# Kernel optimization log

Measured on AMD Instinct MI355X. Metric: run time of the kernel, lower is better.

The kernel has to match this reference:

```python
import jax, jax.numpy as jnp
import numpy as np

B, S, D = 2, 2048, 512
E, K = 8, 2
H = 4 * D  # expert_dim
EPS = 1e-10


def setup_inputs() -> dict:
    key = jax.random.key(0)
    ks = jax.random.split(key, 5)
    scale = 1.0 / np.sqrt(D)
    return {
        "x": jax.random.normal(ks[0], (B, S, D), dtype=jnp.float32),
        "w_router": jax.random.normal(ks[1], (D, E), dtype=jnp.float32) * scale,
        "w_gate": jax.random.normal(ks[2], (D, E * H), dtype=jnp.float32) * scale,
        "w_up": jax.random.normal(ks[3], (D, E * H), dtype=jnp.float32) * scale,
        "w_down": jax.random.normal(ks[4], (H, D), dtype=jnp.float32) * (1.0 / np.sqrt(H)),
    }


def reference(x, w_router, w_gate, w_up, w_down):
    b, s, d = x.shape
    n = b * s
    xf = x.reshape(n, d)

    # Router: softmax over experts, pick top-k, renormalize
    router_probs = jax.nn.softmax(xf @ w_router, axis=-1)          # [N, E]
    top_p, top_i = jax.lax.top_k(router_probs, K)                  # [N, K]
    top_p = top_p / (top_p.sum(axis=-1, keepdims=True) + EPS)

    # Dense all-expert gate/up projections (as in original module)
    gate = jax.nn.silu(xf @ w_gate).reshape(n, E, H)               # [N, E, H]
    up = (xf @ w_up).reshape(n, E, H)                              # [N, E, H]

    # Gather per-token top-k expert slices and combine
    sel_gate = jnp.take_along_axis(gate, top_i[:, :, None], axis=1)  # [N, K, H]
    sel_up = jnp.take_along_axis(up, top_i[:, :, None], axis=1)      # [N, K, H]
    combined = jnp.sum(top_p[:, :, None] * sel_gate * sel_up, axis=1)  # [N, H]

    out = (combined @ w_down).reshape(b, s, d)

    # Load-balancing aux loss
    expert_probs = router_probs.mean(axis=0)                       # [E]
    lb_loss = E * jnp.sum(expert_probs * jnp.log(expert_probs * E + EPS))
    return out, lb_loss
```

## Files before the change

kernel.cpp:

```cpp
#include <hip/hip_runtime.h>
#include <hip/hip_bf16.h>

#define N_TOK 4096
#define D_DIM 512
#define E_NUM 8
#define H_DIM 2048

typedef __attribute__((ext_vector_type(8))) short short8;
typedef __attribute__((ext_vector_type(4))) float f32x4;

__device__ inline short f2bs(float f) {
  __hip_bfloat16 h = __float2bfloat16(f);
  return *reinterpret_cast<short*>(&h);
}

__device__ inline void llds16(const short* g, short* l) {
  __builtin_amdgcn_global_load_lds(
      (const __attribute__((address_space(1))) void*)g,
      (__attribute__((address_space(3))) void*)l, 16, 0, 0);
}

__global__ void __launch_bounds__(256) prep_kernel(
    const float* __restrict__ wg, const float* __restrict__ wu,
    const float* __restrict__ wd, short* __restrict__ wgb,
    short* __restrict__ wub, short* __restrict__ wdb,
    float* __restrict__ out, int* __restrict__ e_cnt,
    float* __restrict__ loss_acc, int* __restrict__ loss_cnt) {
  int u = blockIdx.x;
  int tid = threadIdx.x;
  if (u < 17408) {
    __shared__ float tbuf[32][33];
    const float* in;
    short* op;
    int R, C, c0, r0;
    if (u < 16384) {
      in = (u < 8192) ? wg : wu;
      op = (u < 8192) ? wgb : wub;
      int v = u & 8191;
      R = D_DIM; C = E_NUM * H_DIM;
      c0 = (v & 511) * 32; r0 = (v >> 9) * 32;
    } else {
      in = wd; op = wdb;
      int v = u - 16384;
      R = H_DIM; C = D_DIM;
      c0 = (v & 15) * 32; r0 = (v >> 4) * 32;
    }
    int tx = tid & 31, ty = tid >> 5;
#pragma unroll
    for (int i = 0; i < 4; ++i)
      tbuf[ty + 8 * i][tx] = in[(size_t)(r0 + ty + 8 * i) * C + c0 + tx];
    __syncthreads();
#pragma unroll
    for (int i = 0; i < 4; ++i)
      op[(size_t)(c0 + ty + 8 * i) * R + r0 + tx] = f2bs(tbuf[tx][ty + 8 * i]);
  } else if (u < 17920) {
    int v = u - 17408;
    float4* dst = (float4*)(out + (size_t)v * 4096);
    float4 z = {0.f, 0.f, 0.f, 0.f};
#pragma unroll
    for (int i = 0; i < 4; ++i) dst[tid + 256 * i] = z;
  } else {
    if (tid < 8) { e_cnt[tid] = 0; loss_acc[tid] = 0.f; }
    if (tid == 8) *loss_cnt = 0;
  }
}

__global__ void __launch_bounds__(256) router_kernel(
    const float* __restrict__ x, const float* __restrict__ wr,
    short* __restrict__ xb, int* __restrict__ e_cnt,
    int* __restrict__ e_tok, float* __restrict__ e_p,
    float* __restrict__ loss_acc, int* __restrict__ loss_cnt,
    float* __restrict__ out_loss) {
  __shared__ float wr_lds[D_DIM * E_NUM];
  __shared__ int h_cnt[E_NUM];
  __shared__ int h_base[E_NUM];
  __shared__ float psum[E_NUM];
  int tid = threadIdx.x;

  for (int i = tid; i < D_DIM * E_NUM / 4; i += 256)
    *(float4*)&wr_lds[i * 4] = *(const float4*)&wr[i * 4];
  if (tid < E_NUM) { h_cnt[tid] = 0; psum[tid] = 0.f; }
  __syncthreads();

  int r = tid >> 2, pp = tid & 3;
  int t = blockIdx.x * 64 + r;
  const float* xr = x + (size_t)t * D_DIM + pp * 128;
  short* xw = xb + (size_t)t * D_DIM + pp * 128;
  float acc[8] = {0, 0, 0, 0, 0, 0, 0, 0};
#pragma unroll 4
  for (int j = 0; j < 128; j += 4) {
    float4 xv = *(const float4*)(xr + j);
    short4 o;
    o.x = f2bs(xv.x); o.y = f2bs(xv.y); o.z = f2bs(xv.z); o.w = f2bs(xv.w);
    *(short4*)(xw + j) = o;
    const float* w = &wr_lds[(pp * 128 + j) * E_NUM];
#pragma unroll
    for (int e = 0; e < 8; ++e)
      acc[e] += xv.x * w[e] + xv.y * w[8 + e] + xv.z * w[16 + e] + xv.w * w[24 + e];
  }
#pragma unroll
  for (int e = 0; e < 8; ++e) {
    acc[e] += __shfl_xor(acc[e], 1);
    acc[e] += __shfl_xor(acc[e], 2);
  }

  bool leader = (pp == 0);
  int i0 = 0, i1 = 1, l0 = 0, l1 = 0;
  float q0 = 0.f, q1 = 0.f;
  if (leader) {
    float m = acc[0];
#pragma unroll
    for (int e = 1; e < 8; ++e) m = fmaxf(m, acc[e]);
    float p[8], s = 0.f;
#pragma unroll
    for (int e = 0; e < 8; ++e) { p[e] = expf(acc[e] - m); s += p[e]; }
    float inv = 1.f / s;
#pragma unroll
    for (int e = 0; e < 8; ++e) {
      p[e] *= inv;
      atomicAdd(&psum[e], p[e]);
    }
    i0 = 0;
#pragma unroll
    for (int e = 1; e < 8; ++e) if (p[e] > p[i0]) i0 = e;
    i1 = (i0 == 0) ? 1 : 0;
#pragma unroll
    for (int e = 0; e < 8; ++e) if (e != i0 && p[e] > p[i1]) i1 = e;
    float ps = p[i0] + p[i1] + 1e-10f;
    q0 = p[i0] / ps; q1 = p[i1] / ps;
    l0 = atomicAdd(&h_cnt[i0], 1);
    l1 = atomicAdd(&h_cnt[i1], 1);
  }
  __syncthreads();
  if (tid < E_NUM) {
    h_base[tid] = h_cnt[tid] ? atomicAdd(&e_cnt[tid], h_cnt[tid]) : 0;
    atomicAdd(&loss_acc[tid], psum[tid]);
  }
  __syncthreads();
  if (leader) {
    int s0 = h_base[i0] + l0;
    e_tok[i0 * N_TOK + s0] = t * 2 + 0; e_p[i0 * N_TOK + s0] = q0;
    int s1 = h_base[i1] + l1;
    e_tok[i1 * N_TOK + s1] = t * 2 + 1; e_p[i1 * N_TOK + s1] = q1;
  }
  __threadfence();
  __syncthreads();
  if (tid == 0) {
    int c = atomicAdd(loss_cnt, 1);
    if (c == 63) {
      float lb = 0.f;
#pragma unroll
      for (int e = 0; e < 8; ++e) {
        float pe = atomicAdd(&loss_acc[e], 0.f) / (float)N_TOK;
        lb += pe * logf(pe * 8.f + 1e-10f);
      }
      out_loss[0] = 8.f * lb;
    }
  }
}

__global__ void __launch_bounds__(256, 2) moe_gateup_kernel(
    const short* __restrict__ xb, const short* __restrict__ wg,
    const short* __restrict__ wu, const int* __restrict__ e_cnt,
    const int* __restrict__ e_tok, const float* __restrict__ e_p,
    short* __restrict__ act) {
  __shared__ __align__(16) short As[256 * 64];
  __shared__ __align__(16) short Bgs[64 * 64];
  __shared__ __align__(16) short Bus[64 * 64];
  __shared__ int s_row[256];
  __shared__ float s_pr[256];

  int e = blockIdx.z;
  int n_e = e_cnt[e];
  int rt = blockIdx.y;
  if (rt * 256 >= n_e) return;
  int h0 = blockIdx.x * 64;
  int tid = threadIdx.x;
  int lane = tid & 63, wid = tid >> 6;

  {
    int r = rt * 256 + tid;
    bool v = r < n_e;
    s_row[tid] = v ? e_tok[e * N_TOK + r] : -1;
    s_pr[tid] = v ? e_p[e * N_TOK + r] : 0.f;
  }
  __syncthreads();

  int cg = (lane & 7) ^ (lane >> 3);
  const short* baseA[8];
  const short* baseB[4];
  short* ldsA = As + (size_t)wid * 64 * 64;
  short* ldsB;
#pragma unroll
  for (int jj = 0; jj < 8; ++jj) {
    int r = wid * 64 + jj * 8 + (lane >> 3);
    int row = s_row[r];
    int t = (row < 0) ? 0 : (row >> 1);
    baseA[jj] = xb + (size_t)t * D_DIM + cg * 8;
  }
  {
    const short* wB = ((wid & 2) ? wu : wg) + (size_t)e * H_DIM * D_DIM;
    int rb = (wid & 1) * 32;
    ldsB = ((wid & 2) ? Bus : Bgs) + rb * 64;
#pragma unroll
    for (int jj = 0; jj < 4; ++jj) {
      int h = h0 + rb + jj * 8 + (lane >> 3);
      baseB[jj] = wB + (size_t)h * D_DIM + cg * 8;
    }
  }

  int ml = lane & 15, quad = lane >> 4;
  int m0w = wid * 64;
  f32x4 accG[4][4], accU[4][4];
#pragma unroll
  for (int mf = 0; mf < 4; ++mf)
#pragma unroll
    for (int nf = 0; nf < 4; ++nf) {
      accG[mf][nf] = (f32x4){0, 0, 0, 0};
      accU[mf][nf] = (f32x4){0, 0, 0, 0};
    }

  for (int kt = 0; kt < D_DIM / 64; ++kt) {
    int kb = kt * 64;
#pragma unroll
    for (int jj = 0; jj < 8; ++jj)
      llds16(baseA[jj] + kb, ldsA + jj * 8 * 64);
#pragma unroll
    for (int jj = 0; jj < 4; ++jj)
      llds16(baseB[jj] + kb, ldsB + jj * 8 * 64);
    __syncthreads();
#pragma unroll
    for (int ks = 0; ks < 2; ++ks) {
      int cs = ((quad + ks * 4) ^ (ml & 7)) * 8;
      short8 a[4], bg[4], bu[4];
#pragma unroll
      for (int mf = 0; mf < 4; ++mf)
        a[mf] = *(const short8*)&As[(m0w + mf * 16 + ml) * 64 + cs];
#pragma unroll
      for (int nf = 0; nf < 4; ++nf) {
        bg[nf] = *(const short8*)&Bgs[(nf * 16 + ml) * 64 + cs];
        bu[nf] = *(const short8*)&Bus[(nf * 16 + ml) * 64 + cs];
      }
#pragma unroll
      for (int mf = 0; mf < 4; ++mf)
#pragma unroll
        for (int nf = 0; nf < 4; ++nf) {
          accG[mf][nf] = __builtin_amdgcn_mfma_f32_16x16x32_bf16(a[mf], bg[nf], accG[mf][nf], 0, 0, 0);
          accU[mf][nf] = __builtin_amdgcn_mfma_f32_16x16x32_bf16(a[mf], bu[nf], accU[mf][nf], 0, 0, 0);
        }
    }
    __syncthreads();
  }

#pragma unroll
  for (int mf = 0; mf < 4; ++mf)
#pragma unroll
    for (int r = 0; r < 4; ++r) {
      int rl = m0w + mf * 16 + quad * 4 + r;
      int arow = s_row[rl];
      if (arow >= 0) {
        float pr = s_pr[rl];
#pragma unroll
        for (int nf = 0; nf < 4; ++nf) {
          float g = accG[mf][nf][r], u = accU[mf][nf][r];
          float val = pr * (g / (1.f + __expf(-g))) * u;
          act[(size_t)arow * H_DIM + h0 + nf * 16 + ml] = f2bs(val);
        }
      }
    }
}

__global__ void __launch_bounds__(256, 3) down_kernel(
    const short* __restrict__ act, const short* __restrict__ wd,
    float* __restrict__ out) {
  __shared__ __align__(16) short As[128 * 64];
  __shared__ __align__(16) short Bs[128 * 64];
  int d0 = blockIdx.x * 128;
  int t0 = blockIdx.y * 128;
  int ksb = blockIdx.z;
  int tid = threadIdx.x, lane = tid & 63, wid = tid >> 6;
  int cg = (lane & 7) ^ (lane >> 3);

  const short* baseA[4];
  const short* baseB[4];
  short* ldsA = As + (size_t)wid * 32 * 64;
  short* ldsB = Bs + (size_t)wid * 32 * 64;
#pragma unroll
  for (int jj = 0; jj < 4; ++jj) {
    int r = wid * 32 + jj * 8 + (lane >> 3);
    baseA[jj] = act + (size_t)(2 * (t0 + r)) * H_DIM + cg * 8;
    int d = d0 + wid * 32 + jj * 8 + (lane >> 3);
    baseB[jj] = wd + (size_t)d * H_DIM + cg * 8;
  }

  int ml = lane & 15, quad = lane >> 4;
  int m0w = (wid & 1) * 64, n0w = (wid >> 1) * 64;
  f32x4 acc[4][4];
#pragma unroll
  for (int mf = 0; mf < 4; ++mf)
#pragma unroll
    for (int nf = 0; nf < 4; ++nf) acc[mf][nf] = (f32x4){0, 0, 0, 0};

  for (int kt = ksb * 16; kt < ksb * 16 + 16; ++kt) {
    size_t offA = (size_t)(kt & 1) * H_DIM + (kt >> 1) * 64;
    int offB = (kt >> 1) * 64;
#pragma unroll
    for (int jj = 0; jj < 4; ++jj) {
      llds16(baseA[jj] + offA, ldsA + jj * 8 * 64);
      llds16(baseB[jj] + offB, ldsB + jj * 8 * 64);
    }
    __syncthreads();
#pragma unroll
    for (int ks = 0; ks < 2; ++ks) {
      int cs = ((quad + ks * 4) ^ (ml & 7)) * 8;
      short8 a[4], b[4];
#pragma unroll
      for (int mf = 0; mf < 4; ++mf)
        a[mf] = *(const short8*)&As[(m0w + mf * 16 + ml) * 64 + cs];
#pragma unroll
      for (int nf = 0; nf < 4; ++nf)
        b[nf] = *(const short8*)&Bs[(n0w + nf * 16 + ml) * 64 + cs];
#pragma unroll
      for (int mf = 0; mf < 4; ++mf)
#pragma unroll
        for (int nf = 0; nf < 4; ++nf)
          acc[mf][nf] = __builtin_amdgcn_mfma_f32_16x16x32_bf16(a[mf], b[nf], acc[mf][nf], 0, 0, 0);
    }
    __syncthreads();
  }

#pragma unroll
  for (int mf = 0; mf < 4; ++mf)
#pragma unroll
    for (int r = 0; r < 4; ++r) {
      int t = t0 + m0w + mf * 16 + quad * 4 + r;
#pragma unroll
      for (int nf = 0; nf < 4; ++nf)
        atomicAdd(&out[(size_t)t * D_DIM + d0 + n0w + nf * 16 + ml], acc[mf][nf][r]);
    }
}

extern "C" void kernel_launch(void* const* d_in, const int* in_sizes, int n_in,
                              void* d_out, int out_size, void* d_ws, size_t ws_size,
                              hipStream_t stream) {
  const float* x = (const float*)d_in[0];
  const float* wr = (const float*)d_in[1];
  const float* wg = (const float*)d_in[2];
  const float* wu = (const float*)d_in[3];
  const float* wd = (const float*)d_in[4];
  float* out = (float*)d_out;

  char* ws = (char*)d_ws;
  size_t off = 0;
  auto alloc = [&](size_t bytes) {
    char* p = ws + off;
    off += (bytes + 255) & ~(size_t)255;
    return p;
  };
  short* xb = (short*)alloc((size_t)N_TOK * D_DIM * 2);
  short* wgb = (short*)alloc((size_t)E_NUM * H_DIM * D_DIM * 2);
  short* wub = (short*)alloc((size_t)E_NUM * H_DIM * D_DIM * 2);
  short* wdb = (short*)alloc((size_t)D_DIM * H_DIM * 2);
  short* act = (short*)alloc((size_t)N_TOK * 2 * H_DIM * 2);
  int* e_cnt = (int*)alloc(256);
  int* e_tok = (int*)alloc((size_t)E_NUM * N_TOK * 4);
  float* e_p = (float*)alloc((size_t)E_NUM * N_TOK * 4);
  float* loss_acc = (float*)alloc(256);
  int* loss_cnt = (int*)alloc(256);

  prep_kernel<<<17921, 256, 0, stream>>>(wg, wu, wd, wgb, wub, wdb, out,
                                         e_cnt, loss_acc, loss_cnt);
  router_kernel<<<N_TOK / 64, 256, 0, stream>>>(x, wr, xb, e_cnt, e_tok, e_p,
                                                loss_acc, loss_cnt,
                                                out + (size_t)N_TOK * D_DIM);
  moe_gateup_kernel<<<dim3(H_DIM / 64, N_TOK / 256, E_NUM), 256, 0, stream>>>(
      xb, wgb, wub, e_cnt, e_tok, e_p, act);
  down_kernel<<<dim3(D_DIM / 128, N_TOK / 128, 4), 256, 0, stream>>>(act, wdb, out);
}
```

Before: 247.6 us.

## Replace split-K atomic accumulation with partial buffers and reduce kernel; widen router coalescing

The down projection now writes each split-K slice to its own partial buffer instead of doing float atomicAdds into the output, and a new reduce kernel sums the four slices. This also drops the output-zeroing blocks from the prep kernel. Separately, the router kernel uses 8 threads per token with interleaved, coalesced float4 loads and a padded LDS layout for router weights to avoid bank conflicts, with twice as many blocks. The change trades atomic contention for an extra 32 MB partial write and read plus one more kernel launch.

```diff
diff --git a/kernel.cpp b/kernel.cpp
--- a/kernel.cpp
+++ b/kernel.cpp
@@ -24,8 +24,8 @@
     const float* __restrict__ wg, const float* __restrict__ wu,
     const float* __restrict__ wd, short* __restrict__ wgb,
     short* __restrict__ wub, short* __restrict__ wdb,
-    float* __restrict__ out, int* __restrict__ e_cnt,
-    float* __restrict__ loss_acc, int* __restrict__ loss_cnt) {
+    int* __restrict__ e_cnt, float* __restrict__ loss_acc,
+    int* __restrict__ loss_cnt) {
   int u = blockIdx.x;
   int tid = threadIdx.x;
   if (u < 17408) {
@@ -53,12 +53,6 @@
 #pragma unroll
     for (int i = 0; i < 4; ++i)
       op[(size_t)(c0 + ty + 8 * i) * R + r0 + tx] = f2bs(tbuf[tx][ty + 8 * i]);
-  } else if (u < 17920) {
-    int v = u - 17408;
-    float4* dst = (float4*)(out + (size_t)v * 4096);
-    float4 z = {0.f, 0.f, 0.f, 0.f};
-#pragma unroll
-    for (int i = 0; i < 4; ++i) dst[tid + 256 * i] = z;
   } else {
     if (tid < 8) { e_cnt[tid] = 0; loss_acc[tid] = 0.f; }
     if (tid == 8) *loss_cnt = 0;
@@ -71,37 +65,39 @@
     int* __restrict__ e_tok, float* __restrict__ e_p,
     float* __restrict__ loss_acc, int* __restrict__ loss_cnt,
     float* __restrict__ out_loss) {
-  __shared__ float wr_lds[D_DIM * E_NUM];
+  __shared__ float wr_lds[D_DIM * 9];
   __shared__ int h_cnt[E_NUM];
   __shared__ int h_base[E_NUM];
   __shared__ float psum[E_NUM];
   int tid = threadIdx.x;
 
-  for (int i = tid; i < D_DIM * E_NUM / 4; i += 256)
-    *(float4*)&wr_lds[i * 4] = *(const float4*)&wr[i * 4];
+  for (int i = tid; i < D_DIM * E_NUM; i += 256)
+    wr_lds[(i >> 3) * 9 + (i & 7)] = wr[i];
   if (tid < E_NUM) { h_cnt[tid] = 0; psum[tid] = 0.f; }
   __syncthreads();
 
-  int r = tid >> 2, pp = tid & 3;
-  int t = blockIdx.x * 64 + r;
-  const float* xr = x + (size_t)t * D_DIM + pp * 128;
-  short* xw = xb + (size_t)t * D_DIM + pp * 128;
+  int r = tid >> 3, pp = tid & 7;
+  int t = blockIdx.x * 32 + r;
+  const float* xr0 = x + (size_t)t * D_DIM;
+  short* xw0 = xb + (size_t)t * D_DIM;
   float acc[8] = {0, 0, 0, 0, 0, 0, 0, 0};
 #pragma unroll 4
-  for (int j = 0; j < 128; j += 4) {
-    float4 xv = *(const float4*)(xr + j);
+  for (int j = 0; j < 16; ++j) {
+    int d = j * 32 + pp * 4;
+    float4 xv = *(const float4*)(xr0 + d);
     short4 o;
     o.x = f2bs(xv.x); o.y = f2bs(xv.y); o.z = f2bs(xv.z); o.w = f2bs(xv.w);
-    *(short4*)(xw + j) = o;
-    const float* w = &wr_lds[(pp * 128 + j) * E_NUM];
+    *(short4*)(xw0 + d) = o;
+    const float* w = &wr_lds[d * 9];
 #pragma unroll
     for (int e = 0; e < 8; ++e)
-      acc[e] += xv.x * w[e] + xv.y * w[8 + e] + xv.z * w[16 + e] + xv.w * w[24 + e];
+      acc[e] += xv.x * w[e] + xv.y * w[9 + e] + xv.z * w[18 + e] + xv.w * w[27 + e];
   }
 #pragma unroll
   for (int e = 0; e < 8; ++e) {
     acc[e] += __shfl_xor(acc[e], 1);
     acc[e] += __shfl_xor(acc[e], 2);
+    acc[e] += __shfl_xor(acc[e], 4);
   }
 
   bool leader = (pp == 0);
@@ -147,7 +143,7 @@
   __syncthreads();
   if (tid == 0) {
     int c = atomicAdd(loss_cnt, 1);
-    if (c == 63) {
+    if (c == 127) {
       float lb = 0.f;
 #pragma unroll
       for (int e = 0; e < 8; ++e) {
@@ -272,7 +268,7 @@
 
 __global__ void __launch_bounds__(256, 3) down_kernel(
     const short* __restrict__ act, const short* __restrict__ wd,
-    float* __restrict__ out) {
+    float* __restrict__ partial) {
   __shared__ __align__(16) short As[128 * 64];
   __shared__ __align__(16) short Bs[128 * 64];
   int d0 = blockIdx.x * 128;
@@ -329,6 +325,7 @@
     __syncthreads();
   }
 
+  float* pout = partial + (size_t)ksb * N_TOK * D_DIM;
 #pragma unroll
   for (int mf = 0; mf < 4; ++mf)
 #pragma unroll
@@ -336,8 +333,19 @@
       int t = t0 + m0w + mf * 16 + quad * 4 + r;
 #pragma unroll
       for (int nf = 0; nf < 4; ++nf)
-        atomicAdd(&out[(size_t)t * D_DIM + d0 + n0w + nf * 16 + ml], acc[mf][nf][r]);
-    }
+        pout[(size_t)t * D_DIM + d0 + n0w + nf * 16 + ml] = acc[mf][nf][r];
+    }
+}
+
+__global__ void __launch_bounds__(256) reduce_kernel(
+    const float* __restrict__ partial, float* __restrict__ out) {
+  int i = blockIdx.x * 256 + threadIdx.x;
+  const int Q = N_TOK * D_DIM / 4;
+  const float4* p = (const float4*)partial;
+  float4 a = p[i], b = p[i + Q], c = p[i + 2 * Q], d = p[i + 3 * Q];
+  float4 r = {a.x + b.x + c.x + d.x, a.y + b.y + c.y + d.y,
+              a.z + b.z + c.z + d.z, a.w + b.w + c.w + d.w};
+  ((float4*)out)[i] = r;
 }
 
 extern "C" void kernel_launch(void* const* d_in, const int* in_sizes, int n_in,
@@ -362,18 +370,20 @@
   short* wub = (short*)alloc((size_t)E_NUM * H_DIM * D_DIM * 2);
   short* wdb = (short*)alloc((size_t)D_DIM * H_DIM * 2);
   short* act = (short*)alloc((size_t)N_TOK * 2 * H_DIM * 2);
+  float* partial = (float*)alloc((size_t)4 * N_TOK * D_DIM * 4);
   int* e_cnt = (int*)alloc(256);
   int* e_tok = (int*)alloc((size_t)E_NUM * N_TOK * 4);
   float* e_p = (float*)alloc((size_t)E_NUM * N_TOK * 4);
   float* loss_acc = (float*)alloc(256);
   int* loss_cnt = (int*)alloc(256);
 
-  prep_kernel<<<17921, 256, 0, stream>>>(wg, wu, wd, wgb, wub, wdb, out,
+  prep_kernel<<<17409, 256, 0, stream>>>(wg, wu, wd, wgb, wub, wdb,
                                          e_cnt, loss_acc, loss_cnt);
-  router_kernel<<<N_TOK / 64, 256, 0, stream>>>(x, wr, xb, e_cnt, e_tok, e_p,
+  router_kernel<<<N_TOK / 32, 256, 0, stream>>>(x, wr, xb, e_cnt, e_tok, e_p,
                                                 loss_acc, loss_cnt,
                                                 out + (size_t)N_TOK * D_DIM);
   moe_gateup_kernel<<<dim3(H_DIM / 64, N_TOK / 256, E_NUM), 256, 0, stream>>>(
       xb, wgb, wub, e_cnt, e_tok, e_p, act);
-  down_kernel<<<dim3(D_DIM / 128, N_TOK / 128, 4), 256, 0, stream>>>(act, wdb, out);
-}
+  down_kernel<<<dim3(D_DIM / 128, N_TOK / 128, 4), 256, 0, stream>>>(act, wdb, partial);
+  reduce_kernel<<<N_TOK * D_DIM / 4 / 256, 256, 0, stream>>>(partial, out);
+}
```

New measurement: 242.3 us. -2.1%, faster.
